# Optimization experiments

Measured on AMD Instinct MI355X. Metric: run time of the kernel, lower is better.

Reference implementation:

```python
import jax, jax.numpy as jnp
import numpy as np

K, M, C, P = 3, 64, 1, 7
EPS = 1e-16


def _conv_c(x, w, transpose=False):
    """Complex 2D conv (stride 1, SAME padding) decomposed into 4 real convs.
    x: complex [B,Cin,H,W]; w: complex torch-layout weight.
    transpose=True emulates nn.ConvTranspose2d(M,C,P,stride=1,padding=(P-1)//2):
    weight layout (in=M, out=C, P, P), spatially flipped kernel.
    """
    xr, xi = jnp.real(x), jnp.imag(x)
    wr, wi = jnp.real(w), jnp.imag(w)
    if transpose:
        wr = jnp.flip(wr, (2, 3))
        wi = jnp.flip(wi, (2, 3))
        dn = ('NCHW', 'IOHW', 'NCHW')
    else:
        dn = ('NCHW', 'OIHW', 'NCHW')
    f = lambda a, b: jax.lax.conv_general_dilated(
        a, b, window_strides=(1, 1), padding='SAME', dimension_numbers=dn)
    return jax.lax.complex(f(xr, wr) - f(xi, wi), f(xr, wi) + f(xi, wr))


def _st_complex(x, t):
    """Complex soft-threshold: x * relu(|x| - t) / (|x| + eps)."""
    a = jnp.abs(x)
    return x * (jax.nn.relu(a - t) / (a + EPS))


def setup_inputs() -> dict:
    key = jax.random.key(0)
    ks = jax.random.split(key, 7)
    B, H, W = 4, 256, 256
    wscale = 1.0 / np.sqrt(2.0 * M * P * P)  # keep unrolled loop stable
    return {
        'y_re': jax.random.normal(ks[0], (B, C, H, W), jnp.float32),
        'y_im': jax.random.normal(ks[1], (B, C, H, W), jnp.float32),
        'Aw_re': jax.random.normal(ks[2], (K, M, C, P, P), jnp.float32) * wscale,
        'Aw_im': jax.random.normal(ks[3], (K, M, C, P, P), jnp.float32) * wscale,
        'Bw_re': jax.random.normal(ks[4], (K, M, C, P, P), jnp.float32) * wscale,
        'Bw_im': jax.random.normal(ks[5], (K, M, C, P, P), jnp.float32) * wscale,
        't': jax.random.uniform(ks[6], (K, 2, M, 1, 1), jnp.float32) * 0.01,
    }


def reference(y_re, y_im, Aw_re, Aw_im, Bw_re, Bw_im, t):
    y = jax.lax.complex(y_re, y_im)
    Aw = jax.lax.complex(Aw_re, Aw_im)   # [K,M,C,P,P], Conv2d weights
    Bw = jax.lax.complex(Bw_re, Bw_im)   # [K,M,C,P,P], ConvTranspose2d weights

    # pre_process (stride=1, mask=1): mean-subtract, no padding
    mean = jnp.mean(y, axis=(1, 2, 3), keepdims=True)
    yp = y - mean

    # _lista_core with sigma=None, adaptive=False => c=0, threshold = t[k,0]
    z = _st_complex(_conv_c(yp, Aw[0]), t[0, 0])  # [B,M,H,W] complex
    for k in range(1, K):
        r = _conv_c(z, Bw[k], transpose=True) - yp  # mask == 1
        z = z - _conv_c(r, Aw[k])
        z = _st_complex(z, t[k, 0])

    # decode: D = B[0]; post_process adds mean back
    xhat = _conv_c(z, Bw[0], transpose=True) + mean
    return xhat, z
```

## Files before the change

kernel.cpp:

```cpp
#include <hip/hip_runtime.h>

#define Hh 256
#define Ww 256
#define NB 4
#define NM 64
#define KP 7
#define HW (Hh*Ww)
#define NX (NB*HW)
#define NZQ ((size_t)NB*NM*HW)
#define PT 32
#define TW2 38
#define LDS2T 42
#define NST 6
#define ATY 16
#define ATX 32
#define ATWY 22
#define ATWX 38
#define ALDS 40
#define NTAP (3*NM*49)
#define NSPL 4

typedef unsigned short u16;
typedef unsigned int u32;

__device__ __forceinline__ float bf2f(u16 u) {
  union { u32 i; float f; } c; c.i = ((u32)u) << 16; return c.f;
}
__device__ __forceinline__ u16 f2bf(float f) {
  union { float f; u32 i; } c; c.f = f;
  return (u16)((c.i + 0x7FFFu + ((c.i >> 16) & 1u)) >> 16);
}
__device__ __forceinline__ ushort2 packbf(float x, float y) {
  return make_ushort2(f2bf(x), f2bf(y));
}

__device__ __forceinline__ u32 packh(float x, float y) {
  union { u32 u; _Float16 h[2]; } c;
  c.h[0] = (_Float16)x; c.h[1] = (_Float16)y;
  return c.u;
}
__device__ __forceinline__ float2 unpackh(u32 v) {
  union { u32 u; _Float16 h[2]; } c; c.u = v;
  return make_float2((float)c.h[0], (float)c.h[1]);
}
__device__ __forceinline__ u16 h2bf(u16 hraw) {
  union { u16 u; _Float16 h; } c; c.u = hraw;
  return f2bf((float)c.h);
}

#if __has_builtin(__builtin_amdgcn_fdot2)
typedef _Float16 hf2 __attribute__((ext_vector_type(2)));
__device__ __forceinline__ void cmac2(float& ar, float& ai, u32 v, u32 wre, u32 wim) {
  union { u32 u; hf2 h; } a, b, c;
  a.u = v; b.u = wre; c.u = wim;
  ar = __builtin_amdgcn_fdot2(a.h, b.h, ar, false);
  ai = __builtin_amdgcn_fdot2(a.h, c.h, ai, false);
}
#else
__device__ __forceinline__ void cmac2(float& ar, float& ai, u32 v, u32 wre, u32 wim) {
  float2 a = unpackh(v), b = unpackh(wre), c = unpackh(wim);
  ar = fmaf(a.x, b.x, ar); ar = fmaf(a.y, b.y, ar);
  ai = fmaf(a.x, c.x, ai); ai = fmaf(a.y, c.y, ai);
}
#endif

__device__ __forceinline__ float stfac(float s, float t) {
  return fmaxf(1.f - t*rsqrtf(s), 0.f);
}

__global__ __launch_bounds__(256) void wprep_kernel(
    const float* __restrict__ Awre, const float* __restrict__ Awim,
    const float* __restrict__ Bwre, const float* __restrict__ Bwim,
    uint2* __restrict__ wA, uint2* __restrict__ wB) {
  int i = blockIdx.x*256 + threadIdx.x;
  if (i < NTAP) {
    float wr = Awre[i], wi = Awim[i];
    wA[i] = make_uint2(packh(wr, -wi), packh(wi, wr));
    wr = Bwre[i]; wi = Bwim[i];
    wB[i] = make_uint2(packh(wr, -wi), packh(wi, wr));
  }
}

__global__ __launch_bounds__(256) void mean_stage1(
    const float* __restrict__ yre, const float* __restrict__ yim,
    float2* __restrict__ part) {
  int blk = blockIdx.x;
  int b = blk >> 6, chunk = blk & 63;
  int tid = threadIdx.x;
  int base = b*HW + chunk*1024;
  float sr = 0.f, si = 0.f;
  #pragma unroll
  for (int j = 0; j < 4; ++j) {
    sr += yre[base + tid + j*256];
    si += yim[base + tid + j*256];
  }
  #pragma unroll
  for (int off = 32; off > 0; off >>= 1) {
    sr += __shfl_down(sr, off);
    si += __shfl_down(si, off);
  }
  __shared__ float2 red[4];
  if ((tid & 63) == 0) red[tid >> 6] = make_float2(sr, si);
  __syncthreads();
  if (tid == 0) {
    float2 a = red[0], b2 = red[1], c = red[2], d = red[3];
    part[blk] = make_float2(a.x + b2.x + c.x + d.x, a.y + b2.y + c.y + d.y);
  }
}

__global__ __launch_bounds__(256) void mean_stage2(
    const float2* __restrict__ part, float2* __restrict__ mean) {
  int tid = threadIdx.x;
  int b = tid >> 6, lane = tid & 63;
  float2 v = part[b*64 + lane];
  float sr = v.x, si = v.y;
  #pragma unroll
  for (int off = 32; off > 0; off >>= 1) {
    sr += __shfl_down(sr, off);
    si += __shfl_down(si, off);
  }
  if (lane == 0) mean[b] = make_float2(sr / (float)HW, si / (float)HW);
}

__global__ __launch_bounds__(256) void conv_first_kernel(
    const float* __restrict__ yre, const float* __restrict__ yim,
    const float2* __restrict__ mean,
    const uint2* __restrict__ wA,
    const float* __restrict__ t, u32* __restrict__ z) {
  int tid = threadIdx.x;
  int blk = blockIdx.x;
  int ms  = blk & 3;
  int txi = (blk >> 2) & 7, tyi = (blk >> 5) & 15, b = (blk >> 9) & 3;
  int ty0 = tyi*ATY, tx0 = txi*ATX;
  int thy = tid >> 4, thx = tid & 15;

  __shared__ u32 tile[ATWY][ALDS];
  float2 mb = mean[b];
  const float* re = yre + b*HW;
  const float* im = yim + b*HW;
  for (int i = tid; i < ATWY*ATWX; i += 256) {
    int rr = i / ATWX, cc = i - rr*ATWX;
    int gy = ty0 - 3 + rr, gx = tx0 - 3 + cc;
    u32 v = 0;
    if ((unsigned)gy < Hh && (unsigned)gx < Ww) {
      int o = gy*Ww + gx;
      v = packh(re[o] - mb.x, im[o] - mb.y);
    }
    tile[rr][cc] = v;
  }
  __syncthreads();

  u32* zb = z + ((size_t)b*NM << 16);
  int m0 = ms*16;
  #pragma unroll 1
  for (int mm = 0; mm < 16; mm += 8) {
    int m = m0 + mm;
    const uint2* w0p = wA + m*49;
    float ar[8][2], ai[8][2];
    #pragma unroll
    for (int c = 0; c < 8; ++c) {
      ar[c][0] = 0.f; ar[c][1] = 0.f; ai[c][0] = 0.f; ai[c][1] = 0.f;
    }
    #pragma unroll
    for (int ky = 0; ky < KP; ++ky) {
      #pragma unroll
      for (int kx = 0; kx < KP; ++kx) {
        int wo = ky*KP + kx;
        u32 v0 = tile[thy + ky][thx + kx];
        u32 v1 = tile[thy + ky][thx + 16 + kx];
        #pragma unroll
        for (int c = 0; c < 8; ++c) {
          uint2 w = w0p[c*49 + wo];
          cmac2(ar[c][0], ai[c][0], v0, w.x, w.y);
          cmac2(ar[c][1], ai[c][1], v1, w.x, w.y);
        }
      }
    }
    #pragma unroll
    for (int c = 0; c < 8; ++c) {
      float tc = t[m + c];
      #pragma unroll
      for (int p = 0; p < 2; ++p) {
        size_t o = (size_t)(ty0 + thy)*Ww + tx0 + thx + p*16;
        float s = ar[c][p]*ar[c][p] + ai[c][p]*ai[c][p];
        float f = stfac(s, tc);
        zb[((size_t)(m + c) << 16) + o] = packh(ar[c][p]*f, ai[c][p]*f);
      }
    }
  }
}

__global__ __launch_bounds__(256) void convT_part_kernel(
    const u32* __restrict__ z,
    const uint2* __restrict__ wB,
    int k, float2* __restrict__ rpart) {
  int tid = threadIdx.x;
  int blk = blockIdx.x;
  int s   = blk & 3;
  int txi = (blk >> 2) & 7, tyi = (blk >> 5) & 7, b = (blk >> 8) & 3;
  int ty0 = tyi*PT, tx0 = txi*PT;
  int thy = tid >> 4, thx = tid & 15;

  __shared__ uint4 tile[TW2][LDS2T];

  int srr[NST], scc[NST], soff[NST];
  bool sok[NST], sin[NST];
  #pragma unroll
  for (int j = 0; j < NST; ++j) {
    int i = tid + j*256;
    sin[j] = i < TW2*TW2;
    int rr = sin[j] ? i / TW2 : 0;
    int cc = sin[j] ? i - rr*TW2 : 0;
    int gy = ty0 - 3 + rr, gx = tx0 - 3 + cc;
    sok[j] = sin[j] && (unsigned)gy < Hh && (unsigned)gx < Ww;
    srr[j] = rr; scc[j] = cc;
    soff[j] = sok[j] ? gy*Ww + gx : 0;
  }

  const u32* zb = z + ((size_t)b*NM << 16);
  int m0 = s*16;

  float ar[4] = {0.f,0.f,0.f,0.f}, ai[4] = {0.f,0.f,0.f,0.f};
  #pragma unroll 1
  for (int q = 0; q < 4; ++q) {
    int m = m0 + 4*q;
    if (q) __syncthreads();
    {
      const u32* z0 = zb + ((size_t)m << 16);
      const u32* z1 = zb + ((size_t)(m + 1) << 16);
      const u32* z2 = zb + ((size_t)(m + 2) << 16);
      const u32* z3 = zb + ((size_t)(m + 3) << 16);
      #pragma unroll
      for (int j = 0; j < NST; ++j)
        if (sin[j]) tile[srr[j]][scc[j]] = make_uint4(
          sok[j] ? z0[soff[j]] : 0u, sok[j] ? z1[soff[j]] : 0u,
          sok[j] ? z2[soff[j]] : 0u, sok[j] ? z3[soff[j]] : 0u);
    }
    __syncthreads();

    const uint2* w0p = wB + (k*NM + m)*49;
    #pragma unroll
    for (int ky = 0; ky < KP; ++ky) {
      #pragma unroll
      for (int kx = 0; kx < KP; ++kx) {
        int wo = ky*KP + kx;
        uint2 wa = w0p[wo], wb = w0p[49 + wo], wc = w0p[98 + wo], wd = w0p[147 + wo];
        #pragma unroll
        for (int dy = 0; dy < 2; ++dy) {
          #pragma unroll
          for (int dx = 0; dx < 2; ++dx) {
            uint4 v = tile[thy + dy*16 + 6 - ky][thx + dx*16 + 6 - kx];
            int p = dy*2 + dx;
            cmac2(ar[p], ai[p], v.x, wa.x, wa.y);
            cmac2(ar[p], ai[p], v.y, wb.x, wb.y);
            cmac2(ar[p], ai[p], v.z, wc.x, wc.y);
            cmac2(ar[p], ai[p], v.w, wd.x, wd.y);
          }
        }
      }
    }
  }

  float2* rp = rpart + (size_t)s*NB*HW + (size_t)b*HW;
  #pragma unroll
  for (int dy = 0; dy < 2; ++dy) {
    #pragma unroll
    for (int dx = 0; dx < 2; ++dx) {
      int p = dy*2 + dx;
      int o = (ty0 + thy + dy*16)*Ww + tx0 + thx + dx*16;
      rp[o] = make_float2(ar[p], ai[p]);
    }
  }
}

__global__ __launch_bounds__(256) void rfold_kernel(
    const float2* __restrict__ rpart,
    const float* __restrict__ yre, const float* __restrict__ yim,
    const float2* __restrict__ mean, u32* __restrict__ rq) {
  int p = blockIdx.x*256 + threadIdx.x;
  int b = p >> 16;
  float2 mb = mean[b];
  float2 p0 = rpart[p];
  float2 p1 = rpart[(size_t)NB*HW + p];
  float2 p2 = rpart[(size_t)2*NB*HW + p];
  float2 p3 = rpart[(size_t)3*NB*HW + p];
  rq[p] = packh(p0.x + p1.x + p2.x + p3.x - (yre[p] - mb.x),
                p0.y + p1.y + p2.y + p3.y - (yim[p] - mb.y));
}

__global__ __launch_bounds__(256) void conv_update_kernel(
    const u32* __restrict__ rq,
    const uint2* __restrict__ wA,
    const float* __restrict__ t, int k, u32* __restrict__ z) {
  int tid = threadIdx.x;
  int blk = blockIdx.x;
  int ms  = blk & 3;
  int txi = (blk >> 2) & 7, tyi = (blk >> 5) & 15, b = (blk >> 9) & 3;
  int ty0 = tyi*ATY, tx0 = txi*ATX;
  int thy = tid >> 4, thx = tid & 15;

  __shared__ u32 tile[ATWY][ALDS];
  const u32* rb = rq + b*HW;
  for (int i = tid; i < ATWY*ATWX; i += 256) {
    int rr = i / ATWX, cc = i - rr*ATWX;
    int gy = ty0 - 3 + rr, gx = tx0 - 3 + cc;
    u32 v = 0;
    if ((unsigned)gy < Hh && (unsigned)gx < Ww) v = rb[gy*Ww + gx];
    tile[rr][cc] = v;
  }
  __syncthreads();

  const float* tw = t + k*2*NM;
  u32* zb = z + ((size_t)b*NM << 16);
  int m0 = ms*16;
  #pragma unroll 1
  for (int mm = 0; mm < 16; mm += 8) {
    int m = m0 + mm;
    const uint2* w0p = wA + (k*NM + m)*49;
    float ar[8][2], ai[8][2];
    #pragma unroll
    for (int c = 0; c < 8; ++c) {
      ar[c][0] = 0.f; ar[c][1] = 0.f; ai[c][0] = 0.f; ai[c][1] = 0.f;
    }
    #pragma unroll
    for (int ky = 0; ky < KP; ++ky) {
      #pragma unroll
      for (int kx = 0; kx < KP; ++kx) {
        int wo = ky*KP + kx;
        u32 v0 = tile[thy + ky][thx + kx];
        u32 v1 = tile[thy + ky][thx + 16 + kx];
        #pragma unroll
        for (int c = 0; c < 8; ++c) {
          uint2 w = w0p[c*49 + wo];
          cmac2(ar[c][0], ai[c][0], v0, w.x, w.y);
          cmac2(ar[c][1], ai[c][1], v1, w.x, w.y);
        }
      }
    }
    #pragma unroll
    for (int c = 0; c < 8; ++c) {
      float tc = tw[m + c];
      #pragma unroll
      for (int p = 0; p < 2; ++p) {
        size_t o = (size_t)(ty0 + thy)*Ww + tx0 + thx + p*16;
        size_t q0 = ((size_t)(m + c) << 16) + o;
        float2 z0 = unpackh(zb[q0]);
        float zr0 = z0.x - ar[c][p], zi0 = z0.y - ai[c][p];
        float s = zr0*zr0 + zi0*zi0;
        float f = stfac(s, tc);
        zb[q0] = packh(zr0*f, zi0*f);
      }
    }
  }
}

__global__ __launch_bounds__(256) void xreduce_kernel(
    const float2* __restrict__ xpart,
    const float2* __restrict__ mean, ushort2* __restrict__ xws) {
  int p = blockIdx.x*256 + threadIdx.x;
  int b = p >> 16;
  float2 mb = mean[b];
  float2 a0 = xpart[p];
  float2 a1 = xpart[(size_t)NB*HW + p];
  float2 a2 = xpart[(size_t)2*NB*HW + p];
  float2 a3 = xpart[(size_t)3*NB*HW + p];
  xws[p] = packbf(a0.x + a1.x + a2.x + a3.x + mb.x,
                  a0.y + a1.y + a2.y + a3.y + mb.y);
}

__global__ __launch_bounds__(256) void emit_kernel(
    const ushort2* __restrict__ xws, const u32* __restrict__ zws,
    u16* __restrict__ out16) {
  size_t idx = (size_t)blockIdx.x*256 + threadIdx.x;
  ushort2* out2 = (ushort2*)out16;
  if (idx < (size_t)NX) {
    int p = (int)idx;
    ushort2 xp = xws[p];
    u16 nxt = (p + 1 < NX) ? xws[p + 1].x
                           : h2bf((u16)(zws[0] & 0xffffu));
    out2[p + 1] = make_ushort2(xp.y, nxt);
    if (p == 0) out16[1] = xp.x;
  } else {
    size_t q = idx - (size_t)NX;
    u32 zq = zws[q];
    u16 zim = h2bf((u16)(zq >> 16));
    if (q + 1 < NZQ) {
      u16 zre_next = h2bf((u16)(zws[q + 1] & 0xffffu));
      out2[(size_t)262145 + q] = make_ushort2(zim, zre_next);
    } else {
      out16[(size_t)2*NX + 2*NZQ] = zim;
    }
  }
}

extern "C" void kernel_launch(void* const* d_in, const int* in_sizes, int n_in,
                              void* d_out, int out_size, void* d_ws, size_t ws_size,
                              hipStream_t stream) {
  const float* yre  = (const float*)d_in[0];
  const float* yim  = (const float*)d_in[1];
  const float* Awre = (const float*)d_in[2];
  const float* Awim = (const float*)d_in[3];
  const float* Bwre = (const float*)d_in[4];
  const float* Bwim = (const float*)d_in[5];
  const float* t    = (const float*)d_in[6];

  u32*     zws = (u32*)d_ws;
  ushort2* xws = (ushort2*)((char*)d_ws + (size_t)67108864);

  char* ob = (char*)d_out;
  float2* rpart = (float2*)ob;
  float2* xpart = (float2*)(ob + 8388608);
  float2* mean  = (float2*)(ob + 16777216);
  float2* part  = (float2*)(ob + 16777280);
  uint2*  wA    = (uint2*)(ob + 17825792);
  uint2*  wB    = (uint2*)(ob + 18874368);
  u32*    rq    = (u32*)(ob + 19922944);

  wprep_kernel<<<(NTAP + 255)/256, 256, 0, stream>>>(Awre, Awim, Bwre, Bwim, wA, wB);
  mean_stage1<<<256, 256, 0, stream>>>(yre, yim, part);
  mean_stage2<<<1, 256, 0, stream>>>(part, mean);

  dim3 gridA(NB * (Hh/ATY) * (Ww/ATX) * NSPL);
  dim3 gridT(NB * (Hh/PT) * (Ww/PT) * NSPL);
  conv_first_kernel<<<gridA, 256, 0, stream>>>(yre, yim, mean, wA, t, zws);
  for (int k = 1; k < 3; ++k) {
    convT_part_kernel<<<gridT, 256, 0, stream>>>(zws, wB, k, rpart);
    rfold_kernel<<<NX/256, 256, 0, stream>>>(rpart, yre, yim, mean, rq);
    conv_update_kernel<<<gridA, 256, 0, stream>>>(rq, wA, t, k, zws);
  }
  convT_part_kernel<<<gridT, 256, 0, stream>>>(zws, wB, 0, xpart);
  xreduce_kernel<<<NX/256, 256, 0, stream>>>(xpart, mean, xws);

  size_t total = (size_t)NX + NZQ;
  emit_kernel<<<(unsigned)(total/256), 256, 0, stream>>>(xws, zws, (u16*)d_out);
}
```

Measured before the change: 451.7 us.

## Register-block transposed conv over vertical pixel strip to reuse LDS loads

Changes the convT_part thread mapping so each thread computes 4 vertically adjacent outputs in one column instead of a 2x2 spread. For each kx it loads a 10-row column strip of the LDS tile into registers once and reuses it across all 7 ky taps and 4 outputs. This cuts LDS reads per tap. It costs more vector registers (ten uint4 values live) and could lower occupancy.

```diff
diff --git a/kernel.cpp b/kernel.cpp
--- a/kernel.cpp
+++ b/kernel.cpp
@@ -199,7 +199,8 @@
   int s   = blk & 3;
   int txi = (blk >> 2) & 7, tyi = (blk >> 5) & 7, b = (blk >> 8) & 3;
   int ty0 = tyi*PT, tx0 = txi*PT;
-  int thy = tid >> 4, thx = tid & 15;
+  int thy = tid >> 5;
+  int thx = tid & 31;
 
   __shared__ uint4 tile[TW2][LDS2T];
 
@@ -240,22 +241,22 @@
 
     const uint2* w0p = wB + (k*NM + m)*49;
     #pragma unroll
-    for (int ky = 0; ky < KP; ++ky) {
-      #pragma unroll
-      for (int kx = 0; kx < KP; ++kx) {
+    for (int kx = 0; kx < KP; ++kx) {
+      uint4 v[10];
+      #pragma unroll
+      for (int j = 0; j < 10; ++j)
+        v[j] = tile[4*thy + j][thx + 6 - kx];
+      #pragma unroll
+      for (int ky = 0; ky < KP; ++ky) {
         int wo = ky*KP + kx;
-        uint2 wa = w0p[wo], wb = w0p[49 + wo], wc = w0p[98 + wo], wd = w0p[147 + wo];
+        uint2 wa = w0p[wo], wb2 = w0p[49 + wo], wc = w0p[98 + wo], wd = w0p[147 + wo];
         #pragma unroll
-        for (int dy = 0; dy < 2; ++dy) {
-          #pragma unroll
-          for (int dx = 0; dx < 2; ++dx) {
-            uint4 v = tile[thy + dy*16 + 6 - ky][thx + dx*16 + 6 - kx];
-            int p = dy*2 + dx;
-            cmac2(ar[p], ai[p], v.x, wa.x, wa.y);
-            cmac2(ar[p], ai[p], v.y, wb.x, wb.y);
-            cmac2(ar[p], ai[p], v.z, wc.x, wc.y);
-            cmac2(ar[p], ai[p], v.w, wd.x, wd.y);
-          }
+        for (int p = 0; p < 4; ++p) {
+          uint4 vv = v[p + 6 - ky];
+          cmac2(ar[p], ai[p], vv.x, wa.x, wa.y);
+          cmac2(ar[p], ai[p], vv.y, wb2.x, wb2.y);
+          cmac2(ar[p], ai[p], vv.z, wc.x, wc.y);
+          cmac2(ar[p], ai[p], vv.w, wd.x, wd.y);
         }
       }
     }
@@ -263,13 +264,9 @@
 
   float2* rp = rpart + (size_t)s*NB*HW + (size_t)b*HW;
   #pragma unroll
-  for (int dy = 0; dy < 2; ++dy) {
-    #pragma unroll
-    for (int dx = 0; dx < 2; ++dx) {
-      int p = dy*2 + dx;
-      int o = (ty0 + thy + dy*16)*Ww + tx0 + thx + dx*16;
-      rp[o] = make_float2(ar[p], ai[p]);
-    }
+  for (int p = 0; p < 4; ++p) {
+    int o = (ty0 + 4*thy + p)*Ww + tx0 + thx;
+    rp[o] = make_float2(ar[p], ai[p]);
   }
 }
 
```

After: 509.8 us. 1.13x slower.
